# Optimization experiments

Hardware: AMD Instinct MI355X
Metric: run time of the kernel (lower is better)

## Reference

```python
import jax, jax.numpy as jnp
import numpy as np
from jax import lax

B = 64          # graphs per batch
N0 = 1024       # nodes per graph (equal-sized graphs -> static topk shapes)
DEG = 16        # avg degree
E = B * N0 * DEG
D_IN, D_H, D_OUT = 100, 128, 256
RATIO, EPS = 0.5, 1e-5


def _seg_sum(v, idx, n):
    return jax.ops.segment_sum(v, idx, num_segments=n)


def _gcn(x, src, dst, w_e, W, b, n):
    h = x @ W
    deg = 1.0 + _seg_sum(w_e, dst, n)          # +1 for self-loop
    dinv = lax.rsqrt(deg)
    norm = (dinv[src] * dinv[dst] * w_e)[:, None]
    return _seg_sum(h[src] * norm, dst, n) + h / deg[:, None] + b


def _graphnorm(x, w, bias, ms, nb, k):
    # PyG GraphNorm: per-graph mean/var with learnable mean_scale
    xg = x.reshape(nb, k, -1)
    mean = xg.mean(1, keepdims=True)
    sub = xg - ms * mean
    var = (sub * sub).mean(1, keepdims=True)
    return (w * sub * lax.rsqrt(var + EPS) + bias).reshape(nb * k, -1)


def _topk(x, src, dst, emask, p, nb, n_per):
    # TopKPooling (min_score=None): score = tanh(x.p/||p||), keep top ceil(r*n)
    k = int(np.ceil(RATIO * n_per))
    score = jnp.tanh((x @ p) / jnp.linalg.norm(p))
    vals, idx = lax.top_k(score.reshape(nb, n_per), k)            # [nb, k]
    perm = (idx + (jnp.arange(nb) * n_per)[:, None]).reshape(-1)
    x_new = x[perm] * vals.reshape(-1)[:, None]
    mapping = jnp.full((nb * n_per,), -1, jnp.int32).at[perm].set(
        jnp.arange(nb * k, dtype=jnp.int32))
    ns, nd = mapping[src], mapping[dst]
    valid = emask & (ns >= 0) & (nd >= 0)   # filter_adj as a persistent mask
    return x_new, jnp.where(valid, ns, 0), jnp.where(valid, nd, 0), valid, k


def _forward(x, edge_index, W1, b1, W2, b2, W3, b3,
             gn1_w, gn1_b, gn1_ms, gn2_w, gn2_b, gn2_ms,
             gn3_w, gn3_b, gn3_ms, p1, p2, p3):
    src, dst = edge_index[0], edge_index[1]
    emask = jnp.ones(src.shape, bool)
    Ws, bs = (W1, W2, W3), (b1, b2, b3)
    gw = (gn1_w, gn2_w, gn3_w)
    gb = (gn1_b, gn2_b, gn3_b)
    gm = (gn1_ms, gn2_ms, gn3_ms)
    ps = (p1, p2, p3)
    n_per = N0
    for i in range(3):
        n = B * n_per
        x = _gcn(x, src, dst, emask.astype(x.dtype), Ws[i], bs[i], n)
        x = _graphnorm(x, gw[i], gb[i], gm[i], B, n_per)
        x = jax.nn.relu(x)              # dropout: identity in eval mode
        x, src, dst, emask, n_per = _topk(x, src, dst, emask, ps[i], B, n_per)
    xg = x.reshape(B, n_per, D_OUT)
    # global mean/max pool then concat -> [B, 2*D_OUT]
    return jnp.concatenate([xg.mean(1), xg.max(1)], axis=1)


def setup_inputs():
    key = jax.random.key(0)
    ks = jax.random.split(key, 20)
    x = jax.random.normal(ks[0], (B * N0, D_IN), jnp.float32)
    # random edges within each graph, then offset by graph base index
    e = jax.random.randint(ks[1], (2, B, N0 * DEG), 0, N0, jnp.int32)
    edge_index = (e + (jnp.arange(B, dtype=jnp.int32) * N0)[None, :, None]).reshape(2, -1)
    batch = jnp.repeat(jnp.arange(B, dtype=jnp.int32), N0)
    inp = dict(x=x, edge_index=edge_index, batch=batch)
    dims = [(D_IN, D_H), (D_H, D_H), (D_H, D_OUT)]
    for i, (di, do) in enumerate(dims, 1):
        inp[f"W{i}"] = jax.random.normal(ks[1 + i], (di, do), jnp.float32) / np.sqrt(di)
        inp[f"b{i}"] = jnp.zeros((do,), jnp.float32)
        inp[f"gn{i}_w"] = jnp.ones((do,), jnp.float32)
        inp[f"gn{i}_b"] = jnp.zeros((do,), jnp.float32)
        inp[f"gn{i}_ms"] = jnp.ones((do,), jnp.float32)
        inp[f"p{i}"] = jax.random.normal(ks[10 + i], (do,), jnp.float32)
    return inp


def reference(x, edge_index, batch, W1, b1, W2, b2, W3, b3,
              gn1_w, gn1_b, gn1_ms, gn2_w, gn2_b, gn2_ms,
              gn3_w, gn3_b, gn3_ms, p1, p2, p3):
    del batch  # equal-sized graphs: grouping is encoded by constants B, N0
    return _forward(x, edge_index, W1, b1, W2, b2, W3, b3,
                    gn1_w, gn1_b, gn1_ms, gn2_w, gn2_b, gn2_ms,
                    gn3_w, gn3_b, gn3_ms, p1, p2, p3)
```

## Files before the change

### kernel.cpp

```cpp
#include <hip/hip_runtime.h>

#define GN_EPS 1e-5f

constexpr int NB   = 64;
constexpr int EPG  = 16384;
constexpr int ETOT = NB * EPG;
constexpr int NTOT = 64 * 1024;

__global__ void cmap_init_kernel(int* __restrict__ cmap) {
    int i = blockIdx.x * blockDim.x + threadIdx.x;
    if (i < NTOT) cmap[i] = i;
}

__global__ void compose_map_kernel(int* __restrict__ cmap, const int* __restrict__ mapping) {
    int i = blockIdx.x * blockDim.x + threadIdx.x;
    if (i >= NTOT) return;
    int c = cmap[i];
    cmap[i] = (c >= 0) ? mapping[c] : -1;
}

template <int NPG>
__global__ __launch_bounds__(1024) void csr_build_kernel(
        const int* __restrict__ ei, const int* __restrict__ cmap,
        int* __restrict__ cnt, int* __restrict__ offs, float* __restrict__ dinv,
        int* __restrict__ csr_src) {
    __shared__ int lcnt[NPG];
    __shared__ int lscan[NPG];
    const int g = blockIdx.x;
    const int t = threadIdx.x;
    const int ebase = g * EPG;
    constexpr int EPT = EPG / 1024;

    for (int i = t; i < NPG; i += 1024) lcnt[i] = 0;
    __syncthreads();

    int ms_[EPT], md_[EPT];
#pragma unroll
    for (int i = 0; i < EPT; i++) {
        int e = ebase + t + i * 1024;
        int s = cmap[ei[e]];
        int d = cmap[ei[ETOT + e]];
        bool ok = (s >= 0) && (d >= 0);
        ms_[i] = ok ? s : -1;
        md_[i] = ok ? (d - g * NPG) : 0;
        if (ok) atomicAdd(&lcnt[d - g * NPG], 1);
    }
    __syncthreads();

    if (t < NPG) lscan[t] = lcnt[t];
    __syncthreads();
    for (int d = 1; d < NPG; d <<= 1) {
        int x = 0;
        if (t < NPG && t >= d) x = lscan[t - d];
        __syncthreads();
        if (t < NPG) lscan[t] += x;
        __syncthreads();
    }
    if (t < NPG) {
        int v = lcnt[t];
        int excl = lscan[t] - v;
        cnt[g * NPG + t]  = v;
        offs[g * NPG + t] = ebase + excl;
        dinv[g * NPG + t] = rsqrtf(1.0f + (float)v);
        lcnt[t] = excl;
    }
    __syncthreads();

#pragma unroll
    for (int i = 0; i < EPT; i++) {
        if (ms_[i] >= 0) {
            int pos = atomicAdd(&lcnt[md_[i]], 1);
            csr_src[ebase + pos] = ms_[i];
        }
    }
}

__global__ __launch_bounds__(256) void gemm128_kernel(const float* __restrict__ A,
                                                      const float* __restrict__ W,
                                                      const float* __restrict__ dinv,
                                                      float* __restrict__ C,
                                                      int M, int N, int K) {
    __shared__ float As[16][132];
    __shared__ float Bs[16][132];
    const int bm = blockIdx.x * 128;
    const int bn = blockIdx.y * 128;
    const int tid = threadIdx.x;
    const int tx = tid & 15, ty = tid >> 4;

    const int arow = tid >> 1;
    const int ak   = (tid & 1) * 8;
    const int brow = tid >> 5;
    const int bc4  = (tid & 31) * 4;

    float acc[2][2][4][4] = {};

    for (int k0 = 0; k0 < K; k0 += 16) {
        {
            const float* ap = A + (size_t)(bm + arow) * K + k0 + ak;
            float4 a0 = {0,0,0,0}, a1 = {0,0,0,0};
            if (k0 + ak < K)     a0 = *reinterpret_cast<const float4*>(ap);
            if (k0 + ak + 4 < K) a1 = *reinterpret_cast<const float4*>(ap + 4);
            As[ak + 0][arow] = a0.x; As[ak + 1][arow] = a0.y;
            As[ak + 2][arow] = a0.z; As[ak + 3][arow] = a0.w;
            As[ak + 4][arow] = a1.x; As[ak + 5][arow] = a1.y;
            As[ak + 6][arow] = a1.z; As[ak + 7][arow] = a1.w;
        }
        {
            float4 b0 = {0,0,0,0}, b1 = {0,0,0,0};
            if (k0 + brow < K)
                b0 = *reinterpret_cast<const float4*>(W + (size_t)(k0 + brow) * N + bn + bc4);
            if (k0 + brow + 8 < K)
                b1 = *reinterpret_cast<const float4*>(W + (size_t)(k0 + brow + 8) * N + bn + bc4);
            *reinterpret_cast<float4*>(&Bs[brow][bc4])     = b0;
            *reinterpret_cast<float4*>(&Bs[brow + 8][bc4]) = b1;
        }
        __syncthreads();
#pragma unroll
        for (int k = 0; k < 16; k++) {
            float4 a0 = *reinterpret_cast<const float4*>(&As[k][ty * 4]);
            float4 a1 = *reinterpret_cast<const float4*>(&As[k][64 + ty * 4]);
            float4 b0 = *reinterpret_cast<const float4*>(&Bs[k][tx * 4]);
            float4 b1 = *reinterpret_cast<const float4*>(&Bs[k][64 + tx * 4]);
            const float av[2][4] = {{a0.x, a0.y, a0.z, a0.w}, {a1.x, a1.y, a1.z, a1.w}};
            const float bv[2][4] = {{b0.x, b0.y, b0.z, b0.w}, {b1.x, b1.y, b1.z, b1.w}};
#pragma unroll
            for (int qi = 0; qi < 2; qi++)
#pragma unroll
                for (int qj = 0; qj < 2; qj++)
#pragma unroll
                    for (int i = 0; i < 4; i++)
#pragma unroll
                        for (int j = 0; j < 4; j++)
                            acc[qi][qj][i][j] += av[qi][i] * bv[qj][j];
        }
        __syncthreads();
    }
#pragma unroll
    for (int qi = 0; qi < 2; qi++)
#pragma unroll
        for (int i = 0; i < 4; i++) {
            int row = bm + qi * 64 + ty * 4 + i;
            float dv = dinv[row];
#pragma unroll
            for (int qj = 0; qj < 2; qj++) {
                float4 o = {acc[qi][qj][i][0] * dv, acc[qi][qj][i][1] * dv,
                            acc[qi][qj][i][2] * dv, acc[qi][qj][i][3] * dv};
                *reinterpret_cast<float4*>(&C[(size_t)row * N + bn + qj * 64 + tx * 4]) = o;
            }
        }
}

template <int D4>
__global__ __launch_bounds__(256) void gather_kernel(
        const float* __restrict__ hs, const int* __restrict__ cnt,
        const int* __restrict__ offs, const float* __restrict__ dinv,
        const int* __restrict__ csr_src, const float* __restrict__ b,
        float* __restrict__ out, int n, int bpg) {
    constexpr int NPB = 256 / D4;
    int bid   = blockIdx.x;
    int xcd   = bid & 7;
    int slot  = bid >> 3;
    int graph = xcd + 8 * (slot / bpg);
    int local = slot % bpg;
    int vb    = graph * bpg + local;

    int v  = vb * NPB + threadIdx.x / D4;
    int f4 = threadIdx.x % D4;
    if (v >= n) return;
    const float4* h4 = reinterpret_cast<const float4*>(hs);
    int st = offs[v];
    int c  = cnt[v];
    float4 acc = h4[(size_t)v * D4 + f4];
    int j = 0;
    for (; j + 4 <= c; j += 4) {
        int s0 = csr_src[st + j],     s1 = csr_src[st + j + 1];
        int s2 = csr_src[st + j + 2], s3 = csr_src[st + j + 3];
        float4 h0 = h4[(size_t)s0 * D4 + f4];
        float4 h1 = h4[(size_t)s1 * D4 + f4];
        float4 h2 = h4[(size_t)s2 * D4 + f4];
        float4 h3 = h4[(size_t)s3 * D4 + f4];
        acc.x += h0.x + h1.x + h2.x + h3.x;
        acc.y += h0.y + h1.y + h2.y + h3.y;
        acc.z += h0.z + h1.z + h2.z + h3.z;
        acc.w += h0.w + h1.w + h2.w + h3.w;
    }
    for (; j < c; j++) {
        int s0 = csr_src[st + j];
        float4 h0 = h4[(size_t)s0 * D4 + f4];
        acc.x += h0.x; acc.y += h0.y; acc.z += h0.z; acc.w += h0.w;
    }
    float dv = dinv[v];
    float4 bb = reinterpret_cast<const float4*>(b)[f4];
    float4 o;
    o.x = acc.x * dv + bb.x;
    o.y = acc.y * dv + bb.y;
    o.z = acc.z * dv + bb.z;
    o.w = acc.w * dv + bb.w;
    reinterpret_cast<float4*>(out)[(size_t)v * D4 + f4] = o;
}

template <int D4>
__global__ __launch_bounds__(256) void gn_partial_kernel(
        const float* __restrict__ x, float* __restrict__ sum1, float* __restrict__ sum2,
        int n_per) {
    constexpr int GROUPS = 256 / D4;
    __shared__ float4 l1[256];
    __shared__ float4 l2[256];
    int g = blockIdx.x >> 3;
    int ch = blockIdx.x & 7;
    int f4 = threadIdx.x % D4;
    int grp = threadIdx.x / D4;
    int chunk = n_per / 8;
    int base = g * n_per + ch * chunk;
    const float4* x4 = reinterpret_cast<const float4*>(x);
    float4 s1 = {0.f, 0.f, 0.f, 0.f}, s2 = {0.f, 0.f, 0.f, 0.f};
    for (int i = grp; i < chunk; i += GROUPS) {
        float4 v = x4[(size_t)(base + i) * D4 + f4];
        s1.x += v.x; s1.y += v.y; s1.z += v.z; s1.w += v.w;
        s2.x += v.x * v.x; s2.y += v.y * v.y; s2.z += v.z * v.z; s2.w += v.w * v.w;
    }
    int t = threadIdx.x;
    l1[t] = s1; l2[t] = s2;
    __syncthreads();
    for (int str = 128; str >= D4; str >>= 1) {
        if (t < str) {
            float4 a = l1[t + str], b2 = l2[t + str];
            l1[t].x += a.x; l1[t].y += a.y; l1[t].z += a.z; l1[t].w += a.w;
            l2[t].x += b2.x; l2[t].y += b2.y; l2[t].z += b2.z; l2[t].w += b2.w;
        }
        __syncthreads();
    }
    if (t < D4) {
        size_t slot = (size_t)(g * 8 + ch) * (D4 * 4) + t * 4;
        *reinterpret_cast<float4*>(&sum1[slot]) = l1[t];
        *reinterpret_cast<float4*>(&sum2[slot]) = l2[t];
    }
}

__global__ void gn_final_kernel(const float* __restrict__ sum1, const float* __restrict__ sum2,
                                const float* __restrict__ ms, const float* __restrict__ w,
                                float* __restrict__ cmean, float* __restrict__ srw,
                                int n_per, int D, int total) {
    int t = blockIdx.x * blockDim.x + threadIdx.x;
    if (t >= total) return;
    int g = t / D;
    int f = t % D;
    float s1 = 0.f, s2 = 0.f;
    for (int ch = 0; ch < 8; ch++) {
        size_t slot = (size_t)(g * 8 + ch) * D + f;
        s1 += sum1[slot];
        s2 += sum2[slot];
    }
    float inv_n = 1.0f / (float)n_per;
    float mean = s1 * inv_n;
    float ex2  = s2 * inv_n;
    float m = ms[f];
    float var = ex2 - 2.f * m * mean * mean + m * m * mean * mean;
    cmean[t] = m * mean;
    srw[t]   = w[f] * rsqrtf(var + GN_EPS);
}

__global__ void pnorm3_kernel(const float* __restrict__ p0, const float* __restrict__ p1,
                              const float* __restrict__ p2, int d0, int d1, int d2,
                              float* __restrict__ out) {
    __shared__ float red[256];
    const float* p = (blockIdx.x == 0) ? p0 : (blockIdx.x == 1) ? p1 : p2;
    int d          = (blockIdx.x == 0) ? d0 : (blockIdx.x == 1) ? d1 : d2;
    int t = threadIdx.x;
    float v = (t < d) ? p[t] : 0.0f;
    red[t] = v * v;
    __syncthreads();
    for (int s = 128; s; s >>= 1) {
        if (t < s) red[t] += red[t + s];
        __syncthreads();
    }
    if (t == 0) out[blockIdx.x] = 1.0f / sqrtf(red[0]);
}

template <int DO>
__global__ __launch_bounds__(256) void gn_apply_score_kernel(
        float* __restrict__ x, const float* __restrict__ cmean, const float* __restrict__ srw,
        const float* __restrict__ bias, const float* __restrict__ p,
        const float* __restrict__ pinv, float* __restrict__ score, int n_per) {
    constexpr int V = DO / 64;
    int node = blockIdx.x * 4 + (threadIdx.x >> 6);
    int lane = threadIdx.x & 63;
    int g = node / n_per;
    float*       xr = x + (size_t)node * DO + lane * V;
    const float* cm = cmean + g * DO + lane * V;
    const float* sw = srw + g * DO + lane * V;
    const float* bb = bias + lane * V;
    const float* pp = p + lane * V;
    float dot = 0.f;
#pragma unroll
    for (int i = 0; i < V; i++) {
        float y = (xr[i] - cm[i]) * sw[i] + bb[i];
        y = fmaxf(y, 0.0f);
        xr[i] = y;
        dot += y * pp[i];
    }
#pragma unroll
    for (int off = 32; off; off >>= 1) dot += __shfl_xor(dot, off);
    if (lane == 0) score[node] = tanhf(dot * pinv[0]);
}

template <int N, int K>
__global__ __launch_bounds__(1024) void topk_radix_kernel(
        const float* __restrict__ score, int* __restrict__ mapping,
        int* __restrict__ inv) {
    __shared__ int hist[256];
    __shared__ int sscan[N];
    __shared__ int sbyte, sneed;
    const int g = blockIdx.x;
    const int t = threadIdx.x;
    float sc = score[g * N + t];
    unsigned u = __float_as_uint(sc);
    unsigned key = (u & 0x80000000u) ? ~u : (u | 0x80000000u);

    unsigned prefix = 0;
    int need = K;
#pragma unroll
    for (int shift = 24; shift >= 0; shift -= 8) {
        if (t < 256) hist[t] = 0;
        __syncthreads();
        unsigned hm = (shift == 24) ? 0u : (0xFFFFFFFFu << (shift + 8));
        if ((key & hm) == (prefix & hm))
            atomicAdd(&hist[(key >> shift) & 255], 1);
        __syncthreads();
        if (t < 256) sscan[t] = hist[t];
        __syncthreads();
        for (int d = 1; d < 256; d <<= 1) {
            int x = (t < 256 && t + d < 256) ? sscan[t + d] : 0;
            __syncthreads();
            if (t < 256) sscan[t] += x;
            __syncthreads();
        }
        if (t < 256) {
            int ge  = sscan[t];
            int gt_ = (t + 1 < 256) ? sscan[t + 1] : 0;
            if (ge >= need && gt_ < need) { sbyte = t; sneed = need - gt_; }
        }
        __syncthreads();
        prefix |= ((unsigned)sbyte << shift);
        need = sneed;
        __syncthreads();
    }
    bool gt = key > prefix;
    bool eq = (key == prefix);
    sscan[t] = (gt ? (1 << 16) : 0) | (eq ? 1 : 0);
    __syncthreads();
    for (int d = 1; d < N; d <<= 1) {
        int x = (t >= d) ? sscan[t - d] : 0;
        __syncthreads();
        sscan[t] += x;
        __syncthreads();
    }
    int incl   = sscan[t];
    int gtrank = (incl >> 16) - (gt ? 1 : 0);
    int eqrank = (incl & 0xFFFF) - (eq ? 1 : 0);
    int cntGT  = K - need;
    bool sel = gt || (eq && (eqrank < need));
    int old_g = g * N + t;
    if (sel) {
        int slot = gt ? gtrank : (cntGT + eqrank);
        mapping[old_g] = g * K + slot;
        inv[g * K + slot] = old_g;
    } else {
        mapping[old_g] = -1;
    }
}

__global__ void permute_scale_kernel(const float* __restrict__ x, const int* __restrict__ inv,
                                     const float* __restrict__ score, float* __restrict__ xn,
                                     int total, int ldof4) {
    int t = blockIdx.x * blockDim.x + threadIdx.x;
    if (t >= total) return;
    int node = t >> ldof4;
    int f4   = t & ((1 << ldof4) - 1);
    int dof4 = 1 << ldof4;
    int old = inv[node];
    float sc = score[old];
    float4 v = reinterpret_cast<const float4*>(x)[(size_t)old * dof4 + f4];
    float4 o = {v.x * sc, v.y * sc, v.z * sc, v.w * sc};
    reinterpret_cast<float4*>(xn)[t] = o;
}

__global__ __launch_bounds__(1024) void pool_kernel(const float* __restrict__ x,
                                                    float* __restrict__ out, int n_per) {
    __shared__ float ssum[1024];
    __shared__ float smax[1024];
    int g = blockIdx.x;
    int f = threadIdx.x & 255;
    int ch = threadIdx.x >> 8;
    const float* xg = x + (size_t)g * n_per * 256;
    float s = 0.f, mx = -INFINITY;
    for (int i = ch; i < n_per; i += 4) {
        float v = xg[(size_t)i * 256 + f];
        s += v;
        mx = fmaxf(mx, v);
    }
    ssum[threadIdx.x] = s;
    smax[threadIdx.x] = mx;
    __syncthreads();
    if (ch == 0) {
#pragma unroll
        for (int c = 1; c < 4; c++) {
            s  += ssum[f + c * 256];
            mx  = fmaxf(mx, smax[f + c * 256]);
        }
        out[g * 512 + f]       = s / (float)n_per;
        out[g * 512 + 256 + f] = mx;
    }
}

static inline int cdiv_h(int a, int b) { return (a + b - 1) / b; }

extern "C" void kernel_launch(void* const* d_in, const int* in_sizes, int n_in,
                              void* d_out, int out_size, void* d_ws, size_t ws_size,
                              hipStream_t stream) {
    (void)in_sizes; (void)n_in; (void)out_size; (void)ws_size;

    const float* x_in = (const float*)d_in[0];
    const int*   ei   = (const int*)d_in[1];
    const float* Wm[3]  = {(const float*)d_in[3],  (const float*)d_in[9],  (const float*)d_in[15]};
    const float* bv[3]  = {(const float*)d_in[4],  (const float*)d_in[10], (const float*)d_in[16]};
    const float* gnw[3] = {(const float*)d_in[5],  (const float*)d_in[11], (const float*)d_in[17]};
    const float* gnb[3] = {(const float*)d_in[6],  (const float*)d_in[12], (const float*)d_in[18]};
    const float* gnm[3] = {(const float*)d_in[7],  (const float*)d_in[13], (const float*)d_in[19]};
    const float* pv[3]  = {(const float*)d_in[8],  (const float*)d_in[14], (const float*)d_in[20]};

    size_t off = 0;
    auto alloc = [&](size_t bytes) {
        void* p = (char*)d_ws + off;
        off += (bytes + 255) & ~(size_t)255;
        return p;
    };
    float* X1      = (float*)alloc((size_t)65536 * 128 * 4);
    float* H       = (float*)alloc((size_t)65536 * 128 * 4);
    float* X2      = (float*)alloc((size_t)32768 * 128 * 4);
    int*   csr_src = (int*)alloc((size_t)ETOT * 4);
    int*   cmap    = (int*)alloc(NTOT * 4);
    int*   cnt     = (int*)alloc(65536 * 4);
    int*   offs    = (int*)alloc(65536 * 4);
    float* dinv    = (float*)alloc(65536 * 4);
    float* score   = (float*)alloc(65536 * 4);
    int*   mapping = (int*)alloc(65536 * 4);
    int*   inv     = (int*)alloc(32768 * 4);
    float* sum1    = (float*)alloc(64 * 8 * 256 * 4);
    float* sum2    = (float*)alloc(64 * 8 * 256 * 4);
    float* cmean   = (float*)alloc(64 * 256 * 4);
    float* srw     = (float*)alloc(64 * 256 * 4);
    float* pinv    = (float*)alloc(256);

    const int nper[4] = {1024, 512, 256, 128};
    const int din[3]  = {100, 128, 128};
    const int dof[3]  = {128, 128, 256};

    cmap_init_kernel<<<NTOT / 256, 256, 0, stream>>>(cmap);
    pnorm3_kernel<<<3, 256, 0, stream>>>(pv[0], pv[1], pv[2], dof[0], dof[1], dof[2], pinv);

    for (int L = 0; L < 3; L++) {
        const int n    = NB * nper[L];
        const int k    = nper[L + 1];
        const int nn   = NB * k;
        const int D    = dof[L];
        const int dof4 = D / 4;
        const int ldof4 = (dof4 == 32) ? 5 : 6;
        const float* xin = (L == 0) ? x_in : X2;

        if (nper[L] == 1024)
            csr_build_kernel<1024><<<NB, 1024, 0, stream>>>(ei, cmap, cnt, offs, dinv, csr_src);
        else if (nper[L] == 512)
            csr_build_kernel<512><<<NB, 1024, 0, stream>>>(ei, cmap, cnt, offs, dinv, csr_src);
        else
            csr_build_kernel<256><<<NB, 1024, 0, stream>>>(ei, cmap, cnt, offs, dinv, csr_src);

        gemm128_kernel<<<dim3(n / 128, D / 128), 256, 0, stream>>>(xin, Wm[L], dinv, H,
                                                                   n, D, din[L]);

        if (dof4 == 32) {
            const int NPB = 8;
            const int bpg = nper[L] / NPB;
            gather_kernel<32><<<n / NPB, 256, 0, stream>>>(H, cnt, offs, dinv, csr_src,
                                                           bv[L], X1, n, bpg);
        } else {
            const int NPB = 4;
            const int bpg = nper[L] / NPB;
            gather_kernel<64><<<n / NPB, 256, 0, stream>>>(H, cnt, offs, dinv, csr_src,
                                                           bv[L], X1, n, bpg);
        }

        if (dof4 == 32)
            gn_partial_kernel<32><<<NB * 8, 256, 0, stream>>>(X1, sum1, sum2, nper[L]);
        else
            gn_partial_kernel<64><<<NB * 8, 256, 0, stream>>>(X1, sum1, sum2, nper[L]);
        gn_final_kernel<<<cdiv_h(NB * D, 256), 256, 0, stream>>>(sum1, sum2, gnm[L], gnw[L],
                                                                 cmean, srw, nper[L], D, NB * D);
        if (D == 128)
            gn_apply_score_kernel<128><<<n / 4, 256, 0, stream>>>(X1, cmean, srw, gnb[L],
                                                                  pv[L], pinv + L, score, nper[L]);
        else
            gn_apply_score_kernel<256><<<n / 4, 256, 0, stream>>>(X1, cmean, srw, gnb[L],
                                                                  pv[L], pinv + L, score, nper[L]);

        if (nper[L] == 1024)
            topk_radix_kernel<1024, 512><<<NB, 1024, 0, stream>>>(score, mapping, inv);
        else if (nper[L] == 512)
            topk_radix_kernel<512, 256><<<NB, 512, 0, stream>>>(score, mapping, inv);
        else
            topk_radix_kernel<256, 128><<<NB, 256, 0, stream>>>(score, mapping, inv);

        permute_scale_kernel<<<cdiv_h(nn * dof4, 256), 256, 0, stream>>>(X1, inv, score, X2,
                                                                         nn * dof4, ldof4);
        if (L < 2)
            compose_map_kernel<<<NTOT / 256, 256, 0, stream>>>(cmap, mapping);
    }

    pool_kernel<<<NB, 1024, 0, stream>>>(X2, (float*)d_out, nper[3]);
}
```

Measured before the change: 309.4 us.

## Aggregate before GEMM, fuse GraphNorm finalize, permute+compose, and pooled selection

```diff
diff --git a/kernel.cpp b/kernel.cpp
--- a/kernel.cpp
+++ b/kernel.cpp
@@ -10,13 +10,6 @@
 __global__ void cmap_init_kernel(int* __restrict__ cmap) {
     int i = blockIdx.x * blockDim.x + threadIdx.x;
     if (i < NTOT) cmap[i] = i;
-}
-
-__global__ void compose_map_kernel(int* __restrict__ cmap, const int* __restrict__ mapping) {
-    int i = blockIdx.x * blockDim.x + threadIdx.x;
-    if (i >= NTOT) return;
-    int c = cmap[i];
-    cmap[i] = (c >= 0) ? mapping[c] : -1;
 }
 
 template <int NPG>
@@ -25,7 +18,8 @@
         int* __restrict__ cnt, int* __restrict__ offs, float* __restrict__ dinv,
         int* __restrict__ csr_src) {
     __shared__ int lcnt[NPG];
-    __shared__ int lscan[NPG];
+    __shared__ int wsum[16];
+    constexpr int NW = NPG / 64;
     const int g = blockIdx.x;
     const int t = threadIdx.x;
     const int ebase = g * EPG;
@@ -47,21 +41,33 @@
     }
     __syncthreads();
 
-    if (t < NPG) lscan[t] = lcnt[t];
-    __syncthreads();
-    for (int d = 1; d < NPG; d <<= 1) {
-        int x = 0;
-        if (t < NPG && t >= d) x = lscan[t - d];
-        __syncthreads();
-        if (t < NPG) lscan[t] += x;
-        __syncthreads();
-    }
+    const int lane = t & 63;
+    const int wid  = t >> 6;
+    int orig = (t < NPG) ? lcnt[t] : 0;
+    int v = orig;
+#pragma unroll
+    for (int d = 1; d < 64; d <<= 1) {
+        int u = __shfl_up(v, d);
+        if (lane >= d) v += u;
+    }
+    if (lane == 63) wsum[wid] = v;
+    __syncthreads();
+    if (wid == 0) {
+        int wv = (lane < NW) ? wsum[lane] : 0;
+#pragma unroll
+        for (int d = 1; d < 16; d <<= 1) {
+            int u = __shfl_up(wv, d);
+            if (lane >= d) wv += u;
+        }
+        if (lane < NW) wsum[lane] = wv;
+    }
+    __syncthreads();
     if (t < NPG) {
-        int v = lcnt[t];
-        int excl = lscan[t] - v;
-        cnt[g * NPG + t]  = v;
+        int incl = v + ((wid > 0) ? wsum[wid - 1] : 0);
+        int excl = incl - orig;
+        cnt[g * NPG + t]  = orig;
         offs[g * NPG + t] = ebase + excl;
-        dinv[g * NPG + t] = rsqrtf(1.0f + (float)v);
+        dinv[g * NPG + t] = rsqrtf(1.0f + (float)orig);
         lcnt[t] = excl;
     }
     __syncthreads();
@@ -75,9 +81,57 @@
     }
 }
 
+template <int D4, int NPB>
+__global__ __launch_bounds__(256) void gather_kernel(
+        const float* __restrict__ x, const int* __restrict__ cnt,
+        const int* __restrict__ offs, const float* __restrict__ dinv,
+        const int* __restrict__ csr_src, float* __restrict__ z, int n, int bpg) {
+    int bid   = blockIdx.x;
+    int xcd   = bid & 7;
+    int slot  = bid >> 3;
+    int graph = xcd + 8 * (slot / bpg);
+    int local = slot % bpg;
+    int vb    = graph * bpg + local;
+
+    int grp = threadIdx.x / D4;
+    int f4  = threadIdx.x % D4;
+    if (grp >= NPB) return;
+    int v = vb * NPB + grp;
+    if (v >= n) return;
+
+    const float4* x4 = reinterpret_cast<const float4*>(x);
+    int st = offs[v];
+    int c  = cnt[v];
+    float dv = dinv[v];
+    float4 xv = x4[(size_t)v * D4 + f4];
+    float4 acc = {xv.x * dv, xv.y * dv, xv.z * dv, xv.w * dv};
+    int j = 0;
+    for (; j + 4 <= c; j += 4) {
+        int s0 = csr_src[st + j],     s1 = csr_src[st + j + 1];
+        int s2 = csr_src[st + j + 2], s3 = csr_src[st + j + 3];
+        float d0 = dinv[s0], d1 = dinv[s1], d2 = dinv[s2], d3 = dinv[s3];
+        float4 h0 = x4[(size_t)s0 * D4 + f4];
+        float4 h1 = x4[(size_t)s1 * D4 + f4];
+        float4 h2 = x4[(size_t)s2 * D4 + f4];
+        float4 h3 = x4[(size_t)s3 * D4 + f4];
+        acc.x += h0.x * d0 + h1.x * d1 + h2.x * d2 + h3.x * d3;
+        acc.y += h0.y * d0 + h1.y * d1 + h2.y * d2 + h3.y * d3;
+        acc.z += h0.z * d0 + h1.z * d1 + h2.z * d2 + h3.z * d3;
+        acc.w += h0.w * d0 + h1.w * d1 + h2.w * d2 + h3.w * d3;
+    }
+    for (; j < c; j++) {
+        int s0 = csr_src[st + j];
+        float d0 = dinv[s0];
+        float4 h0 = x4[(size_t)s0 * D4 + f4];
+        acc.x += h0.x * d0; acc.y += h0.y * d0; acc.z += h0.z * d0; acc.w += h0.w * d0;
+    }
+    float4 o = {acc.x * dv, acc.y * dv, acc.z * dv, acc.w * dv};
+    reinterpret_cast<float4*>(z)[(size_t)v * D4 + f4] = o;
+}
+
 __global__ __launch_bounds__(256) void gemm128_kernel(const float* __restrict__ A,
                                                       const float* __restrict__ W,
-                                                      const float* __restrict__ dinv,
+                                                      const float* __restrict__ Bias,
                                                       float* __restrict__ C,
                                                       int M, int N, int K) {
     __shared__ float As[16][132];
@@ -135,68 +189,21 @@
         }
         __syncthreads();
     }
+    float4 bb[2];
+    bb[0] = *reinterpret_cast<const float4*>(&Bias[bn + tx * 4]);
+    bb[1] = *reinterpret_cast<const float4*>(&Bias[bn + 64 + tx * 4]);
 #pragma unroll
     for (int qi = 0; qi < 2; qi++)
 #pragma unroll
         for (int i = 0; i < 4; i++) {
             int row = bm + qi * 64 + ty * 4 + i;
-            float dv = dinv[row];
 #pragma unroll
             for (int qj = 0; qj < 2; qj++) {
-                float4 o = {acc[qi][qj][i][0] * dv, acc[qi][qj][i][1] * dv,
-                            acc[qi][qj][i][2] * dv, acc[qi][qj][i][3] * dv};
+                float4 o = {acc[qi][qj][i][0] + bb[qj].x, acc[qi][qj][i][1] + bb[qj].y,
+                            acc[qi][qj][i][2] + bb[qj].z, acc[qi][qj][i][3] + bb[qj].w};
                 *reinterpret_cast<float4*>(&C[(size_t)row * N + bn + qj * 64 + tx * 4]) = o;
             }
         }
-}
-
-template <int D4>
-__global__ __launch_bounds__(256) void gather_kernel(
-        const float* __restrict__ hs, const int* __restrict__ cnt,
-        const int* __restrict__ offs, const float* __restrict__ dinv,
-        const int* __restrict__ csr_src, const float* __restrict__ b,
-        float* __restrict__ out, int n, int bpg) {
-    constexpr int NPB = 256 / D4;
-    int bid   = blockIdx.x;
-    int xcd   = bid & 7;
-    int slot  = bid >> 3;
-    int graph = xcd + 8 * (slot / bpg);
-    int local = slot % bpg;
-    int vb    = graph * bpg + local;
-
-    int v  = vb * NPB + threadIdx.x / D4;
-    int f4 = threadIdx.x % D4;
-    if (v >= n) return;
-    const float4* h4 = reinterpret_cast<const float4*>(hs);
-    int st = offs[v];
-    int c  = cnt[v];
-    float4 acc = h4[(size_t)v * D4 + f4];
-    int j = 0;
-    for (; j + 4 <= c; j += 4) {
-        int s0 = csr_src[st + j],     s1 = csr_src[st + j + 1];
-        int s2 = csr_src[st + j + 2], s3 = csr_src[st + j + 3];
-        float4 h0 = h4[(size_t)s0 * D4 + f4];
-        float4 h1 = h4[(size_t)s1 * D4 + f4];
-        float4 h2 = h4[(size_t)s2 * D4 + f4];
-        float4 h3 = h4[(size_t)s3 * D4 + f4];
-        acc.x += h0.x + h1.x + h2.x + h3.x;
-        acc.y += h0.y + h1.y + h2.y + h3.y;
-        acc.z += h0.z + h1.z + h2.z + h3.z;
-        acc.w += h0.w + h1.w + h2.w + h3.w;
-    }
-    for (; j < c; j++) {
-        int s0 = csr_src[st + j];
-        float4 h0 = h4[(size_t)s0 * D4 + f4];
-        acc.x += h0.x; acc.y += h0.y; acc.z += h0.z; acc.w += h0.w;
-    }
-    float dv = dinv[v];
-    float4 bb = reinterpret_cast<const float4*>(b)[f4];
-    float4 o;
-    o.x = acc.x * dv + bb.x;
-    o.y = acc.y * dv + bb.y;
-    o.z = acc.z * dv + bb.z;
-    o.w = acc.w * dv + bb.w;
-    reinterpret_cast<float4*>(out)[(size_t)v * D4 + f4] = o;
 }
 
 template <int D4>
@@ -237,29 +244,6 @@
     }
 }
 
-__global__ void gn_final_kernel(const float* __restrict__ sum1, const float* __restrict__ sum2,
-                                const float* __restrict__ ms, const float* __restrict__ w,
-                                float* __restrict__ cmean, float* __restrict__ srw,
-                                int n_per, int D, int total) {
-    int t = blockIdx.x * blockDim.x + threadIdx.x;
-    if (t >= total) return;
-    int g = t / D;
-    int f = t % D;
-    float s1 = 0.f, s2 = 0.f;
-    for (int ch = 0; ch < 8; ch++) {
-        size_t slot = (size_t)(g * 8 + ch) * D + f;
-        s1 += sum1[slot];
-        s2 += sum2[slot];
-    }
-    float inv_n = 1.0f / (float)n_per;
-    float mean = s1 * inv_n;
-    float ex2  = s2 * inv_n;
-    float m = ms[f];
-    float var = ex2 - 2.f * m * mean * mean + m * m * mean * mean;
-    cmean[t] = m * mean;
-    srw[t]   = w[f] * rsqrtf(var + GN_EPS);
-}
-
 __global__ void pnorm3_kernel(const float* __restrict__ p0, const float* __restrict__ p1,
                               const float* __restrict__ p2, int d0, int d1, int d2,
                               float* __restrict__ out) {
@@ -279,22 +263,41 @@
 
 template <int DO>
 __global__ __launch_bounds__(256) void gn_apply_score_kernel(
-        float* __restrict__ x, const float* __restrict__ cmean, const float* __restrict__ srw,
+        float* __restrict__ x, const float* __restrict__ sum1, const float* __restrict__ sum2,
+        const float* __restrict__ ms, const float* __restrict__ w,
         const float* __restrict__ bias, const float* __restrict__ p,
         const float* __restrict__ pinv, float* __restrict__ score, int n_per) {
     constexpr int V = DO / 64;
+    __shared__ float scm[DO];
+    __shared__ float ssr[DO];
     int node = blockIdx.x * 4 + (threadIdx.x >> 6);
     int lane = threadIdx.x & 63;
     int g = node / n_per;
+    float inv_n = 1.0f / (float)n_per;
+    for (int f = threadIdx.x; f < DO; f += 256) {
+        float s1 = 0.f, s2 = 0.f;
+#pragma unroll
+        for (int ch = 0; ch < 8; ch++) {
+            s1 += sum1[(size_t)(g * 8 + ch) * DO + f];
+            s2 += sum2[(size_t)(g * 8 + ch) * DO + f];
+        }
+        float mean = s1 * inv_n;
+        float ex2  = s2 * inv_n;
+        float m = ms[f];
+        float var = ex2 - 2.f * m * mean * mean + m * m * mean * mean;
+        scm[f] = m * mean;
+        ssr[f] = w[f] * rsqrtf(var + GN_EPS);
+    }
+    __syncthreads();
+
     float*       xr = x + (size_t)node * DO + lane * V;
-    const float* cm = cmean + g * DO + lane * V;
-    const float* sw = srw + g * DO + lane * V;
     const float* bb = bias + lane * V;
     const float* pp = p + lane * V;
     float dot = 0.f;
 #pragma unroll
     for (int i = 0; i < V; i++) {
-        float y = (xr[i] - cm[i]) * sw[i] + bb[i];
+        int f = lane * V + i;
+        float y = (xr[i] - scm[f]) * ssr[f] + bb[i];
         y = fmaxf(y, 0.0f);
         xr[i] = y;
         dot += y * pp[i];
@@ -370,32 +373,41 @@
     }
 }
 
-__global__ void permute_scale_kernel(const float* __restrict__ x, const int* __restrict__ inv,
-                                     const float* __restrict__ score, float* __restrict__ xn,
-                                     int total, int ldof4) {
+__global__ void permute_compose_kernel(const float* __restrict__ x, const int* __restrict__ inv,
+                                       const float* __restrict__ score, float* __restrict__ xn,
+                                       int total, int ldof4,
+                                       int* __restrict__ cmap, const int* __restrict__ mapping) {
     int t = blockIdx.x * blockDim.x + threadIdx.x;
-    if (t >= total) return;
-    int node = t >> ldof4;
-    int f4   = t & ((1 << ldof4) - 1);
-    int dof4 = 1 << ldof4;
-    int old = inv[node];
-    float sc = score[old];
-    float4 v = reinterpret_cast<const float4*>(x)[(size_t)old * dof4 + f4];
-    float4 o = {v.x * sc, v.y * sc, v.z * sc, v.w * sc};
-    reinterpret_cast<float4*>(xn)[t] = o;
-}
-
-__global__ __launch_bounds__(1024) void pool_kernel(const float* __restrict__ x,
-                                                    float* __restrict__ out, int n_per) {
+    if (t < total) {
+        int node = t >> ldof4;
+        int f4   = t & ((1 << ldof4) - 1);
+        int dof4 = 1 << ldof4;
+        int old = inv[node];
+        float sc = score[old];
+        float4 v = reinterpret_cast<const float4*>(x)[(size_t)old * dof4 + f4];
+        float4 o = {v.x * sc, v.y * sc, v.z * sc, v.w * sc};
+        reinterpret_cast<float4*>(xn)[t] = o;
+    }
+    if (t < NTOT) {
+        int c = cmap[t];
+        cmap[t] = (c >= 0) ? mapping[c] : -1;
+    }
+}
+
+__global__ __launch_bounds__(1024) void pool_sel_kernel(const float* __restrict__ x,
+                                                        const int* __restrict__ inv,
+                                                        const float* __restrict__ score,
+                                                        float* __restrict__ out) {
     __shared__ float ssum[1024];
     __shared__ float smax[1024];
     int g = blockIdx.x;
     int f = threadIdx.x & 255;
     int ch = threadIdx.x >> 8;
-    const float* xg = x + (size_t)g * n_per * 256;
     float s = 0.f, mx = -INFINITY;
-    for (int i = ch; i < n_per; i += 4) {
-        float v = xg[(size_t)i * 256 + f];
+    for (int i = ch; i < 128; i += 4) {
+        int old = inv[g * 128 + i];
+        float sc = score[old];
+        float v = x[(size_t)old * 256 + f] * sc;
         s += v;
         mx = fmaxf(mx, v);
     }
@@ -408,7 +420,7 @@
             s  += ssum[f + c * 256];
             mx  = fmaxf(mx, smax[f + c * 256]);
         }
-        out[g * 512 + f]       = s / (float)n_per;
+        out[g * 512 + f]       = s / 128.0f;
         out[g * 512 + 256 + f] = mx;
     }
 }
@@ -436,7 +448,7 @@
         return p;
     };
     float* X1      = (float*)alloc((size_t)65536 * 128 * 4);
-    float* H       = (float*)alloc((size_t)65536 * 128 * 4);
+    float* Z       = (float*)alloc((size_t)65536 * 128 * 4);
     float* X2      = (float*)alloc((size_t)32768 * 128 * 4);
     int*   csr_src = (int*)alloc((size_t)ETOT * 4);
     int*   cmap    = (int*)alloc(NTOT * 4);
@@ -448,8 +460,6 @@
     int*   inv     = (int*)alloc(32768 * 4);
     float* sum1    = (float*)alloc(64 * 8 * 256 * 4);
     float* sum2    = (float*)alloc(64 * 8 * 256 * 4);
-    float* cmean   = (float*)alloc(64 * 256 * 4);
-    float* srw     = (float*)alloc(64 * 256 * 4);
     float* pinv    = (float*)alloc(256);
 
     const int nper[4] = {1024, 512, 256, 128};
@@ -475,33 +485,33 @@
         else
             csr_build_kernel<256><<<NB, 1024, 0, stream>>>(ei, cmap, cnt, offs, dinv, csr_src);
 
-        gemm128_kernel<<<dim3(n / 128, D / 128), 256, 0, stream>>>(xin, Wm[L], dinv, H,
-                                                                   n, D, din[L]);
-
-        if (dof4 == 32) {
+        {
             const int NPB = 8;
             const int bpg = nper[L] / NPB;
-            gather_kernel<32><<<n / NPB, 256, 0, stream>>>(H, cnt, offs, dinv, csr_src,
-                                                           bv[L], X1, n, bpg);
-        } else {
-            const int NPB = 4;
-            const int bpg = nper[L] / NPB;
-            gather_kernel<64><<<n / NPB, 256, 0, stream>>>(H, cnt, offs, dinv, csr_src,
-                                                           bv[L], X1, n, bpg);
-        }
+            if (L == 0)
+                gather_kernel<25, 8><<<n / NPB, 256, 0, stream>>>(xin, cnt, offs, dinv,
+                                                                  csr_src, Z, n, bpg);
+            else
+                gather_kernel<32, 8><<<n / NPB, 256, 0, stream>>>(xin, cnt, offs, dinv,
+                                                                  csr_src, Z, n, bpg);
+        }
+
+        gemm128_kernel<<<dim3(n / 128, D / 128), 256, 0, stream>>>(Z, Wm[L], bv[L], X1,
+                                                                   n, D, din[L]);
 
         if (dof4 == 32)
             gn_partial_kernel<32><<<NB * 8, 256, 0, stream>>>(X1, sum1, sum2, nper[L]);
         else
             gn_partial_kernel<64><<<NB * 8, 256, 0, stream>>>(X1, sum1, sum2, nper[L]);
-        gn_final_kernel<<<cdiv_h(NB * D, 256), 256, 0, stream>>>(sum1, sum2, gnm[L], gnw[L],
-                                                                 cmean, srw, nper[L], D, NB * D);
+
         if (D == 128)
-            gn_apply_score_kernel<128><<<n / 4, 256, 0, stream>>>(X1, cmean, srw, gnb[L],
-                                                                  pv[L], pinv + L, score, nper[L]);
+            gn_apply_score_kernel<128><<<n / 4, 256, 0, stream>>>(X1, sum1, sum2, gnm[L],
+                                                                  gnw[L], gnb[L], pv[L],
+                                                                  pinv + L, score, nper[L]);
         else
-            gn_apply_score_kernel<256><<<n / 4, 256, 0, stream>>>(X1, cmean, srw, gnb[L],
-                                                                  pv[L], pinv + L, score, nper[L]);
+            gn_apply_score_kernel<256><<<n / 4, 256, 0, stream>>>(X1, sum1, sum2, gnm[L],
+                                                                  gnw[L], gnb[L], pv[L],
+                                                                  pinv + L, score, nper[L]);
 
         if (nper[L] == 1024)
             topk_radix_kernel<1024, 512><<<NB, 1024, 0, stream>>>(score, mapping, inv);
@@ -510,11 +520,12 @@
         else
             topk_radix_kernel<256, 128><<<NB, 256, 0, stream>>>(score, mapping, inv);
 
-        permute_scale_kernel<<<cdiv_h(nn * dof4, 256), 256, 0, stream>>>(X1, inv, score, X2,
-                                                                         nn * dof4, ldof4);
-        if (L < 2)
-            compose_map_kernel<<<NTOT / 256, 256, 0, stream>>>(cmap, mapping);
-    }
-
-    pool_kernel<<<NB, 1024, 0, stream>>>(X2, (float*)d_out, nper[3]);
-}
+        if (L < 2) {
+            int total = nn * dof4;
+            permute_compose_kernel<<<cdiv_h(total, 256), 256, 0, stream>>>(
+                X1, inv, score, X2, total, ldof4, cmap, mapping);
+        } else {
+            pool_sel_kernel<<<NB, 1024, 0, stream>>>(X1, inv, score, (float*)d_out);
+        }
+    }
+}
```

New measurement: 311.9 us. About the same (+0.8%).
